# Performance work log

Hardware: AMD Instinct MI355X
Metric: run time of the kernel (lower is better)

The kernel has to match this reference:

```python
import jax, jax.numpy as jnp
import numpy as np

N_ITER = 3


def squash(v):
    # v: [..., out_C]; scale by ||v||^2/(1+||v||^2) and normalize by ||v||
    sq = jnp.sum(v * v, axis=-1, keepdims=True)
    return (sq / (1.0 + sq)) * v / jnp.sqrt(sq)


def setup_inputs() -> dict:
    key = jax.random.key(0)
    k1, k2 = jax.random.split(key)
    B, n_nodes, n_caps, in_C, out_C = 64, 2048, 32, 16, 32
    x = jax.random.normal(k1, (B, n_nodes, in_C), dtype=jnp.float32)
    route_weights = 0.1 * jax.random.normal(k2, (n_nodes, n_caps, in_C, out_C), dtype=jnp.float32)
    return {"x": x, "route_weights": route_weights}


def reference(x, route_weights):
    # priors: [B, n_nodes, n_caps, out_C]
    priors = jnp.einsum('bni,nkio->bnko', x, route_weights)
    logits = jnp.zeros_like(priors)
    outputs = None
    for i in range(N_ITER):
        probs = jax.nn.softmax(logits, axis=2)            # over n_caps
        s = jnp.sum(probs * priors, axis=1, keepdims=True)  # [B,1,n_caps,out_C]
        outputs = squash(s)
        if i != N_ITER - 1:
            delta = jnp.sum(priors * outputs, axis=-1, keepdims=True)
            logits = logits + delta
    return outputs
```

## Files before the change

kernel.cpp:

```cpp
#include <hip/hip_runtime.h>
#include <math.h>


#define BATCH 64
#define NN    2048
#define NK    32
#define NI    16
#define NO    32

#define PNB   16
#define NSETS (NN / PNB)
#define NCH   4
#define XT_JS 528
#define XT0_JS 1040

typedef __bf16 bf16x8 __attribute__((ext_vector_type(8)));
typedef float  f32x16 __attribute__((ext_vector_type(16)));

__device__ __forceinline__ unsigned short f2bf(float f) {
    unsigned int x = __float_as_uint(f);
    unsigned int lsb = (x >> 16) & 1u;
    x += 0x7fffu + lsb;
    return (unsigned short)(x >> 16);
}
__device__ __forceinline__ float bflo(unsigned int u) { return __uint_as_float(u << 16); }
__device__ __forceinline__ float bfhi(unsigned int u) { return __uint_as_float(u & 0xffff0000u); }

__global__ __launch_bounds__(1024) void pass0_fused(
    const float* __restrict__ xg,
    const float* __restrict__ Wg,
    unsigned short* __restrict__ wq,
    float* __restrict__ part)
{
    __shared__ unsigned short xt_lds[PNB * XT0_JS];

    const int tid   = threadIdx.x;
    const int w     = tid >> 6;
    const int lane  = tid & 63;
    const int l5    = lane & 31;
    const int h5    = lane >> 5;
    const int set   = blockIdx.x;
    const int khalf = blockIdx.y;
    const int k     = khalf * 16 + w;
    const int nbase = set * PNB;

#pragma unroll
    for (int rr = 0; rr < 4; ++rr) {
        const int id  = tid + rr * 1024;
        const int bl  = id >> 6;
        const int rem = id & 63;
        const int j   = rem >> 2;
        const int i4  = rem & 3;
        float4 v = *(const float4*)(xg + ((size_t)bl * NN + (nbase + j)) * NI + i4 * 4);
        ushort4 o4;
        o4.x = f2bf(v.x); o4.y = f2bf(v.y); o4.z = f2bf(v.z); o4.w = f2bf(v.w);
        *(ushort4*)(xt_lds + j * XT0_JS + bl * 16 + i4 * 4) = o4;
    }
    __syncthreads();

    float sa0[16], sa1[16];
#pragma unroll
    for (int r = 0; r < 16; ++r) { sa0[r] = 0.f; sa1[r] = 0.f; }

    float wf[8];
    {
        const float* wsrc = Wg + ((size_t)nbase * NK + k) * (NI * NO) + h5 * 8 * NO + l5;
#pragma unroll
        for (int jj = 0; jj < 8; ++jj)
            wf[jj] = wsrc[jj * NO];
    }

    for (int j = 0; j < PNB; ++j) {
        const int n = nbase + j;
        float wfn[8];
        if (j < PNB - 1) {
            const float* wsrcN = Wg + ((size_t)(n + 1) * NK + k) * (NI * NO) + h5 * 8 * NO + l5;
#pragma unroll
            for (int jj = 0; jj < 8; ++jj)
                wfn[jj] = wsrcN[jj * NO];
        }

        unsigned short us[8];
#pragma unroll
        for (int jj = 0; jj < 8; ++jj)
            us[jj] = f2bf(wf[jj]);
        *(uint4*)(wq + ((size_t)n * NK + k) * (NO * NI) + l5 * NI + h5 * 8) = *(uint4*)us;
        const bf16x8 bC = *(const bf16x8*)us;

        const bf16x8 aA = *(const bf16x8*)(xt_lds + j * XT0_JS + l5 * 16 + h5 * 8);
        const bf16x8 aB = *(const bf16x8*)(xt_lds + j * XT0_JS + 512 + l5 * 16 + h5 * 8);

        f32x16 c0, c1;
#pragma unroll
        for (int r = 0; r < 16; ++r) { c0[r] = 0.f; c1[r] = 0.f; }
        c0 = __builtin_amdgcn_mfma_f32_32x32x16_bf16(bC, aA, c0, 0, 0, 0);
        c1 = __builtin_amdgcn_mfma_f32_32x32x16_bf16(bC, aB, c1, 0, 0, 0);
#pragma unroll
        for (int r = 0; r < 16; ++r) { sa0[r] += c0[r]; sa1[r] += c1[r]; }

        if (j < PNB - 1) {
#pragma unroll
            for (int jj = 0; jj < 8; ++jj)
                wf[jj] = wfn[jj];
        }
    }

    float* pb = part + ((size_t)(khalf * NSETS + set) << 15);
#pragma unroll
    for (int r = 0; r < 16; ++r) {
        const int o = (r & 3) + 8 * (r >> 2) + 4 * h5;
        pb[(w * NO + o) * 64 + l5]      = sa0[r] * (1.f / NK);
        pb[(w * NO + o) * 64 + 32 + l5] = sa1[r] * (1.f / NK);
    }
}

template <int PASS>
__global__ __launch_bounds__(1024) void fused_pass(
    const float* __restrict__ xg,
    const unsigned short* __restrict__ wq,
    const float* __restrict__ vpart,
    float* __restrict__ logits0,
    float* __restrict__ part)
{
    __shared__ unsigned short xt_lds[PNB * XT_JS];
    __shared__ float delta_lds[2][32 * 33];

    const int tid  = threadIdx.x;
    const int w    = tid >> 6;
    const int lane = tid & 63;
    const int l5   = lane & 31;
    const int h5   = lane >> 5;
    const int set  = blockIdx.x;
    const int hb   = blockIdx.y;
    const int k0   = 2 * w, k1 = 2 * w + 1;
    const int gb5  = hb * 32 + l5;
    const int sb   = tid >> 5;
    const int sk   = tid & 31;
    const int nbase = set * PNB;

#pragma unroll
    for (int rr = 0; rr < 2; ++rr) {
        const int id  = tid + rr * 1024;
        const int bl  = id >> 6;
        const int rem = id & 63;
        const int j   = rem >> 2;
        const int i4  = rem & 3;
        float4 v = *(const float4*)(xg + ((size_t)(hb * 32 + bl) * NN + (nbase + j)) * NI + i4 * 4);
        ushort4 o4;
        o4.x = f2bf(v.x); o4.y = f2bf(v.y); o4.z = f2bf(v.z); o4.w = f2bf(v.w);
        *(ushort4*)(xt_lds + j * XT_JS + bl * 16 + i4 * 4) = o4;
    }
    __syncthreads();

    unsigned orp0[8], orp1[8];
    {
        float v0[16], v1[16];
        float sq0 = 0.f, sq1 = 0.f;
#pragma unroll
        for (int r = 0; r < 16; ++r) {
            const int o = (r & 3) + 8 * (r >> 2) + 4 * h5;
            float a = 0.f, b = 0.f;
#pragma unroll
            for (int c = 0; c < NCH; ++c) {
                a += vpart[(((size_t)c * NK + k0) * NO + o) * BATCH + gb5];
                b += vpart[(((size_t)c * NK + k1) * NO + o) * BATCH + gb5];
            }
            v0[r] = a; v1[r] = b;
            sq0 = fmaf(a, a, sq0);
            sq1 = fmaf(b, b, sq1);
        }
        sq0 += __shfl_xor(sq0, 32);
        sq1 += __shfl_xor(sq1, 32);
        const float cf0 = sq0 / ((1.f + sq0) * sqrtf(sq0));
        const float cf1 = sq1 / ((1.f + sq1) * sqrtf(sq1));
#pragma unroll
        for (int q = 0; q < 8; ++q) {
            orp0[q] = (unsigned)f2bf(v0[2 * q] * cf0) | ((unsigned)f2bf(v0[2 * q + 1] * cf0) << 16);
            orp1[q] = (unsigned)f2bf(v1[2 * q] * cf1) | ((unsigned)f2bf(v1[2 * q + 1] * cf1) << 16);
        }
    }

    float sa0[16], sa1[16];
#pragma unroll
    for (int r = 0; r < 16; ++r) { sa0[r] = 0.f; sa1[r] = 0.f; }

    bf16x8 b0N, b1N;
    float gN = 0.f;
    {
        const int n = nbase;
        b0N = *(const bf16x8*)(wq + (size_t)n * (NK * NO * NI) + k0 * (NO * NI) + l5 * NI + h5 * 8);
        b1N = *(const bf16x8*)(wq + (size_t)n * (NK * NO * NI) + k1 * (NO * NI) + l5 * NI + h5 * 8);
        if constexpr (PASS == 2)
            gN = logits0[(size_t)n * (BATCH * NK) + hb * 1024 + tid];
    }

    int buf = 0;
    for (int j = 0; j < PNB; ++j) {
        const int n = nbase + j;
        const bf16x8 b0C = b0N, b1C = b1N;
        const float gC = gN;
        if (j < PNB - 1) {
            const int n2 = n + 1;
            b0N = *(const bf16x8*)(wq + (size_t)n2 * (NK * NO * NI) + k0 * (NO * NI) + l5 * NI + h5 * 8);
            b1N = *(const bf16x8*)(wq + (size_t)n2 * (NK * NO * NI) + k1 * (NO * NI) + l5 * NI + h5 * 8);
            if constexpr (PASS == 2)
                gN = logits0[(size_t)n2 * (BATCH * NK) + hb * 1024 + tid];
        }
        const bf16x8 aC = *(const bf16x8*)(xt_lds + j * XT_JS + l5 * 16 + h5 * 8);

        f32x16 c0, c1;
#pragma unroll
        for (int r = 0; r < 16; ++r) { c0[r] = 0.f; c1[r] = 0.f; }
        c0 = __builtin_amdgcn_mfma_f32_32x32x16_bf16(b0C, aC, c0, 0, 0, 0);
        c1 = __builtin_amdgcn_mfma_f32_32x32x16_bf16(b1C, aC, c1, 0, 0, 0);

        float d0 = 0.f, d1 = 0.f;
#pragma unroll
        for (int r = 0; r < 16; ++r) {
            const unsigned u0 = orp0[r >> 1], u1 = orp1[r >> 1];
            const float o0 = (r & 1) ? bfhi(u0) : bflo(u0);
            const float o1 = (r & 1) ? bfhi(u1) : bflo(u1);
            d0 = fmaf(c0[r], o0, d0);
            d1 = fmaf(c1[r], o1, d1);
        }
        d0 += __shfl_xor(d0, 32);
        d1 += __shfl_xor(d1, 32);

        delta_lds[buf][l5 * 33 + (h5 ? k1 : k0)] = h5 ? d1 : d0;
        __syncthreads();

        float l = delta_lds[buf][sb * 33 + sk];
        if constexpr (PASS == 1)
            logits0[(size_t)n * (BATCH * NK) + hb * 1024 + tid] = l;
        else
            l += gC;
        float e = __expf(l);
        float s = e;
#pragma unroll
        for (int mask = 1; mask < 32; mask <<= 1)
            s += __shfl_xor(s, mask);
        delta_lds[buf][sb * 33 + sk] = e / s;
        __syncthreads();

        const float p0 = delta_lds[buf][l5 * 33 + k0];
        const float p1 = delta_lds[buf][l5 * 33 + k1];
#pragma unroll
        for (int r = 0; r < 16; ++r) {
            sa0[r] = fmaf(p0, c0[r], sa0[r]);
            sa1[r] = fmaf(p1, c1[r], sa1[r]);
        }
        buf ^= 1;
    }

    float* pb = part + ((size_t)(hb * NSETS + set) << 15);
#pragma unroll
    for (int r = 0; r < 16; ++r) {
        const int o = (r & 3) + 8 * (r >> 2) + 4 * h5;
        pb[(k0 * NO + o) * 32 + l5] = sa0[r];
        pb[(k1 * NO + o) * 32 + l5] = sa1[r];
    }
}

__global__ __launch_bounds__(1024) void reduce_stageA(
    const float* __restrict__ part,
    float* __restrict__ vpart)
{
    const int k  = blockIdx.x;
    const int hb = blockIdx.y;
    const int c  = blockIdx.z;
    const int t  = threadIdx.x;
    const int o  = t >> 5;
    const int b  = t & 31;

    const float* src = part + ((size_t)(hb * NSETS + c * (NSETS / NCH)) << 15)
                            + (k << 10) + (o << 5) + b;
    float v0 = 0.f, v1 = 0.f, v2 = 0.f, v3 = 0.f;
#pragma unroll 4
    for (int s = 0; s < NSETS / NCH; s += 4) {
        v0 += src[(size_t)(s + 0) << 15];
        v1 += src[(size_t)(s + 1) << 15];
        v2 += src[(size_t)(s + 2) << 15];
        v3 += src[(size_t)(s + 3) << 15];
    }
    vpart[(((size_t)c * NK + k) * NO + o) * BATCH + hb * 32 + b] = (v0 + v1) + (v2 + v3);
}

__global__ __launch_bounds__(1024) void reduce_stageA0(
    const float* __restrict__ part,
    float* __restrict__ vpart)
{
    const int k  = blockIdx.x;
    const int hb = blockIdx.y;
    const int c  = blockIdx.z;
    const int t  = threadIdx.x;
    const int o  = t >> 5;
    const int b  = t & 31;
    const int khalf = k >> 4, kk = k & 15;

    const float* src = part + ((size_t)(khalf * NSETS + c * (NSETS / NCH)) << 15)
                            + ((kk * NO + o) << 6) + hb * 32 + b;
    float v0 = 0.f, v1 = 0.f, v2 = 0.f, v3 = 0.f;
#pragma unroll 4
    for (int s = 0; s < NSETS / NCH; s += 4) {
        v0 += src[(size_t)(s + 0) << 15];
        v1 += src[(size_t)(s + 1) << 15];
        v2 += src[(size_t)(s + 2) << 15];
        v3 += src[(size_t)(s + 3) << 15];
    }
    vpart[(((size_t)c * NK + k) * NO + o) * BATCH + hb * 32 + b] = (v0 + v1) + (v2 + v3);
}

__global__ __launch_bounds__(1024) void reduce_final(
    const float* __restrict__ vpart,
    float* __restrict__ outp)
{
    __shared__ float s_lds[32 * 33];
    __shared__ float cf_lds[32];
    const int k  = blockIdx.x;
    const int hb = blockIdx.y;
    const int t  = threadIdx.x;
    const int o  = t >> 5;
    const int b  = t & 31;

    float v = 0.f;
#pragma unroll
    for (int c = 0; c < NCH; ++c)
        v += vpart[(((size_t)c * NK + k) * NO + o) * BATCH + hb * 32 + b];
    s_lds[o * 33 + b] = v;
    __syncthreads();
    if (t < 32) {
        float sq = 0.f;
#pragma unroll
        for (int oo = 0; oo < 32; ++oo) { const float x = s_lds[oo * 33 + t]; sq = fmaf(x, x, sq); }
        cf_lds[t] = sq / ((1.f + sq) * sqrtf(sq));
    }
    __syncthreads();
    const int bq = t >> 5, oq = t & 31;
    outp[(size_t)(hb * 32 + bq) * 1024 + k * 32 + oq] = s_lds[oq * 33 + bq] * cf_lds[bq];
}


#define LBB 32
#define LNCHUNK 8
#define LNBLK (NN / LNCHUNK)
#define LTHREADS 512
#define WK_STRIDE 516

template <int PASS>
__global__ __launch_bounds__(LTHREADS, 1) void legacy_pass(
    const float* __restrict__ xg, const float* __restrict__ Wg,
    const float* __restrict__ outvL, float* __restrict__ logits,
    float* __restrict__ partial)
{
    __shared__ float w_lds[NK * WK_STRIDE];
    __shared__ float x_lds[LBB][NI + 1];
    __shared__ float delta_lds[LBB][NK + 1];
    const int t = threadIdx.x, nb = blockIdx.x, bg = blockIdx.y;
    const int b0 = bg * LBB;
    const int k = t >> 4, bq = t & 15, bl0 = bq * 2, bl1 = bq * 2 + 1;
    float acc0[NO], acc1[NO];
#pragma unroll
    for (int o = 0; o < NO; ++o) { acc0[o] = 0.f; acc1[o] = 0.f; }
    float outr0[NO], outr1[NO];
    if constexpr (PASS >= 1) {
        const float4* o0 = (const float4*)&outvL[((b0 + bl0) * NK + k) * NO];
        const float4* o1 = (const float4*)&outvL[((b0 + bl1) * NK + k) * NO];
#pragma unroll
        for (int q = 0; q < NO / 4; ++q) {
            float4 a = o0[q]; float4 b = o1[q];
            outr0[4*q+0]=a.x; outr0[4*q+1]=a.y; outr0[4*q+2]=a.z; outr0[4*q+3]=a.w;
            outr1[4*q+0]=b.x; outr1[4*q+1]=b.y; outr1[4*q+2]=b.z; outr1[4*q+3]=b.w;
        }
    }
    for (int j = 0; j < LNCHUNK; ++j) {
        const int n = nb * LNCHUNK + j;
        __syncthreads();
        {
            const float4* src = (const float4*)(Wg + (size_t)n * (NK * NI * NO));
#pragma unroll
            for (int r = 0; r < (NK * NI * NO / 4) / LTHREADS; ++r) {
                int idx4 = t + r * LTHREADS;
                float4 v = src[idx4];
                int e = idx4 * 4, kk = e >> 9, rem = e & 511;
                *(float4*)&w_lds[kk * WK_STRIDE + rem] = v;
            }
        }
        { int bl = t >> 4, i = t & 15;
          x_lds[bl][i] = xg[((size_t)(b0 + bl) * NN + n) * NI + i]; }
        __syncthreads();
        if constexpr (PASS == 0) {
#pragma unroll
            for (int i = 0; i < NI; ++i) {
                float xa = x_lds[bl0][i], xb = x_lds[bl1][i];
                const float* wrow = &w_lds[k * WK_STRIDE + i * NO];
#pragma unroll
                for (int o = 0; o < NO; ++o) {
                    float w = wrow[o];
                    acc0[o] = fmaf(xa, w, acc0[o]);
                    acc1[o] = fmaf(xb, w, acc1[o]);
                }
            }
        } else {
            float pr0[NO], pr1[NO];
#pragma unroll
            for (int o = 0; o < NO; ++o) { pr0[o] = 0.f; pr1[o] = 0.f; }
#pragma unroll
            for (int i = 0; i < NI; ++i) {
                float xa = x_lds[bl0][i], xb = x_lds[bl1][i];
                const float* wrow = &w_lds[k * WK_STRIDE + i * NO];
#pragma unroll
                for (int o = 0; o < NO; ++o) {
                    float w = wrow[o];
                    pr0[o] = fmaf(xa, w, pr0[o]);
                    pr1[o] = fmaf(xb, w, pr1[o]);
                }
            }
            float d0 = 0.f, d1 = 0.f;
#pragma unroll
            for (int o = 0; o < NO; ++o) {
                d0 = fmaf(pr0[o], outr0[o], d0);
                d1 = fmaf(pr1[o], outr1[o], d1);
            }
            float l0 = d0, l1 = d1;
            const size_t li0 = ((size_t)(b0 + bl0) * NN + n) * NK + k;
            const size_t li1 = ((size_t)(b0 + bl1) * NN + n) * NK + k;
            if constexpr (PASS == 2) { l0 += logits[li0]; l1 += logits[li1]; }
            else { logits[li0] = d0; logits[li1] = d1; }
            delta_lds[bl0][k] = l0; delta_lds[bl1][k] = l1;
            __syncthreads();
            float m0 = -1e30f, m1 = -1e30f;
#pragma unroll
            for (int kk = 0; kk < NK; ++kk) {
                m0 = fmaxf(m0, delta_lds[bl0][kk]);
                m1 = fmaxf(m1, delta_lds[bl1][kk]);
            }
            float s0 = 0.f, s1 = 0.f;
#pragma unroll
            for (int kk = 0; kk < NK; ++kk) {
                s0 += __expf(delta_lds[bl0][kk] - m0);
                s1 += __expf(delta_lds[bl1][kk] - m1);
            }
            float p0 = __expf(l0 - m0) / s0;
            float p1 = __expf(l1 - m1) / s1;
#pragma unroll
            for (int o = 0; o < NO; ++o) {
                acc0[o] = fmaf(p0, pr0[o], acc0[o]);
                acc1[o] = fmaf(p1, pr1[o], acc1[o]);
            }
        }
    }
    const float scale = (PASS == 0) ? (1.f / NK) : 1.f;
    float4* p0 = (float4*)&partial[(((size_t)nb * BATCH + (b0 + bl0)) * NK + k) * NO];
    float4* p1 = (float4*)&partial[(((size_t)nb * BATCH + (b0 + bl1)) * NK + k) * NO];
#pragma unroll
    for (int q = 0; q < NO / 4; ++q) {
        float4 v0, v1;
        v0.x = acc0[4*q+0]*scale; v0.y = acc0[4*q+1]*scale;
        v0.z = acc0[4*q+2]*scale; v0.w = acc0[4*q+3]*scale;
        v1.x = acc1[4*q+0]*scale; v1.y = acc1[4*q+1]*scale;
        v1.z = acc1[4*q+2]*scale; v1.w = acc1[4*q+3]*scale;
        p0[q] = v0; p1[q] = v1;
    }
}

__global__ __launch_bounds__(256) void legacy_reduce(
    const float* __restrict__ partial, float* __restrict__ outf)
{
    const int tid = blockIdx.x * 256 + threadIdx.x;
    float v = 0.f;
    for (int nb = 0; nb < LNBLK; ++nb)
        v += partial[(size_t)nb * (BATCH * NK * NO) + tid];
    float sq = v * v;
#pragma unroll
    for (int off = 1; off < 32; off <<= 1) sq += __shfl_xor(sq, off);
    float coef = sq / ((1.f + sq) * sqrtf(sq));
    outf[tid] = v * coef;
}


extern "C" void kernel_launch(void* const* d_in, const int* in_sizes, int n_in,
                              void* d_out, int out_size, void* d_ws, size_t ws_size,
                              hipStream_t stream)
{
    const float* xg = (const float*)d_in[0];
    const float* Wg = (const float*)d_in[1];
    float* outp = (float*)d_out;
    char* ws = (char*)d_ws;

    const size_t SZ_WQ     = (size_t)NN * NK * NO * NI * 2;
    const size_t SZ_PART   = (size_t)256 * 32768 * 4;
    const size_t SZ_LOGITS = (size_t)NN * BATCH * NK * 4;
    const size_t SZ_VPART  = (size_t)NCH * NK * NO * BATCH * 4;
    const size_t NEED = SZ_WQ + SZ_PART + SZ_LOGITS + SZ_VPART;

    if (ws_size >= NEED) {
        unsigned short* wq = (unsigned short*)ws;
        float* part    = (float*)(ws + SZ_WQ);
        float* logits0 = (float*)(ws + SZ_WQ + SZ_PART);
        float* vpart   = (float*)(ws + SZ_WQ + SZ_PART + SZ_LOGITS);

        dim3 pg(NSETS, 2);
        dim3 ra(NK, 2, NCH);
        dim3 fg(NK, 2);
        pass0_fused<<<pg, 1024, 0, stream>>>(xg, Wg, wq, part);
        reduce_stageA0<<<ra, 1024, 0, stream>>>(part, vpart);
        fused_pass<1><<<pg, 1024, 0, stream>>>(xg, wq, vpart, logits0, part);
        reduce_stageA<<<ra, 1024, 0, stream>>>(part, vpart);
        fused_pass<2><<<pg, 1024, 0, stream>>>(xg, wq, vpart, logits0, part);
        reduce_stageA<<<ra, 1024, 0, stream>>>(part, vpart);
        reduce_final<<<fg, 1024, 0, stream>>>(vpart, outp);
    } else {
        float* partial = (float*)ws;
        float* logits = (float*)(ws + (size_t)LNBLK * BATCH * NK * NO * 4);
        float* outvL = (float*)(ws + (size_t)LNBLK * BATCH * NK * NO * 4 + (size_t)BATCH * NN * NK * 4);
        dim3 grid(LNBLK, BATCH / LBB);
        const int rblocks = BATCH * NK * NO / 256;
        legacy_pass<0><<<grid, LTHREADS, 0, stream>>>(xg, Wg, nullptr, logits, partial);
        legacy_reduce<<<rblocks, 256, 0, stream>>>(partial, outvL);
        legacy_pass<1><<<grid, LTHREADS, 0, stream>>>(xg, Wg, outvL, logits, partial);
        legacy_reduce<<<rblocks, 256, 0, stream>>>(partial, outvL);
        legacy_pass<2><<<grid, LTHREADS, 0, stream>>>(xg, Wg, outvL, logits, partial);
        legacy_reduce<<<rblocks, 256, 0, stream>>>(partial, outp);
    }
}
```

Measured before the change: 320.9 us.

## Fuse all routing passes into one persistent kernel with grid barriers

Replaces the seven kernel launches (pass0, reductions, two routing passes, final squash) with a single persistent kernel of 256 blocks that synchronises between stages using atomic grid barriers in workspace memory. The x tile is converted to bf16 and staged in LDS once and reused across all passes, so the per-pass reload goes away. This is meant to cut launch gaps and redundant x loads, at the cost of spin-wait barrier overhead, a reliance on all 256 blocks being co-resident, and an extra memset launch.

```diff
diff --git a/kernel.cpp b/kernel.cpp
--- a/kernel.cpp
+++ b/kernel.cpp
@@ -11,7 +11,7 @@
 #define PNB   16
 #define NSETS (NN / PNB)
 #define NCH   4
-#define XT_JS 528
+#define NBLK  256
 #define XT0_JS 1040
 
 typedef __bf16 bf16x8 __attribute__((ext_vector_type(8)));
@@ -26,22 +26,38 @@
 __device__ __forceinline__ float bflo(unsigned int u) { return __uint_as_float(u << 16); }
 __device__ __forceinline__ float bfhi(unsigned int u) { return __uint_as_float(u & 0xffff0000u); }
 
-__global__ __launch_bounds__(1024) void pass0_fused(
+__device__ __forceinline__ void grid_bar(unsigned* __restrict__ bar, int idx) {
+    __syncthreads();
+    if (threadIdx.x == 0) {
+        __builtin_amdgcn_fence(__ATOMIC_RELEASE, "agent");
+        __hip_atomic_fetch_add(&bar[idx], 1u, __ATOMIC_RELAXED, __HIP_MEMORY_SCOPE_AGENT);
+        while (__hip_atomic_load(&bar[idx], __ATOMIC_RELAXED, __HIP_MEMORY_SCOPE_AGENT) < NBLK)
+            __builtin_amdgcn_s_sleep(2);
+        __builtin_amdgcn_fence(__ATOMIC_ACQUIRE, "agent");
+    }
+    __syncthreads();
+}
+
+__global__ __launch_bounds__(1024) void routing_mega(
     const float* __restrict__ xg,
     const float* __restrict__ Wg,
     unsigned short* __restrict__ wq,
-    float* __restrict__ part)
+    float* __restrict__ part,
+    float* __restrict__ logits0,
+    float* __restrict__ vpart,
+    unsigned* __restrict__ bar,
+    float* __restrict__ outp)
 {
     __shared__ unsigned short xt_lds[PNB * XT0_JS];
-
-    const int tid   = threadIdx.x;
-    const int w     = tid >> 6;
-    const int lane  = tid & 63;
-    const int l5    = lane & 31;
-    const int h5    = lane >> 5;
-    const int set   = blockIdx.x;
-    const int khalf = blockIdx.y;
-    const int k     = khalf * 16 + w;
+    __shared__ float delta_lds[2][32 * 33];
+
+    const int tid  = threadIdx.x;
+    const int bid  = blockIdx.x;
+    const int w    = tid >> 6;
+    const int lane = tid & 63;
+    const int l5   = lane & 31;
+    const int h5   = lane >> 5;
+    const int set  = bid & 127;
     const int nbase = set * PNB;
 
 #pragma unroll
@@ -58,285 +74,248 @@
     }
     __syncthreads();
 
-    float sa0[16], sa1[16];
-#pragma unroll
-    for (int r = 0; r < 16; ++r) { sa0[r] = 0.f; sa1[r] = 0.f; }
-
-    float wf[8];
     {
-        const float* wsrc = Wg + ((size_t)nbase * NK + k) * (NI * NO) + h5 * 8 * NO + l5;
-#pragma unroll
-        for (int jj = 0; jj < 8; ++jj)
-            wf[jj] = wsrc[jj * NO];
-    }
-
-    for (int j = 0; j < PNB; ++j) {
-        const int n = nbase + j;
-        float wfn[8];
-        if (j < PNB - 1) {
-            const float* wsrcN = Wg + ((size_t)(n + 1) * NK + k) * (NI * NO) + h5 * 8 * NO + l5;
-#pragma unroll
-            for (int jj = 0; jj < 8; ++jj)
-                wfn[jj] = wsrcN[jj * NO];
-        }
-
-        unsigned short us[8];
-#pragma unroll
-        for (int jj = 0; jj < 8; ++jj)
-            us[jj] = f2bf(wf[jj]);
-        *(uint4*)(wq + ((size_t)n * NK + k) * (NO * NI) + l5 * NI + h5 * 8) = *(uint4*)us;
-        const bf16x8 bC = *(const bf16x8*)us;
-
-        const bf16x8 aA = *(const bf16x8*)(xt_lds + j * XT0_JS + l5 * 16 + h5 * 8);
-        const bf16x8 aB = *(const bf16x8*)(xt_lds + j * XT0_JS + 512 + l5 * 16 + h5 * 8);
-
-        f32x16 c0, c1;
-#pragma unroll
-        for (int r = 0; r < 16; ++r) { c0[r] = 0.f; c1[r] = 0.f; }
-        c0 = __builtin_amdgcn_mfma_f32_32x32x16_bf16(bC, aA, c0, 0, 0, 0);
-        c1 = __builtin_amdgcn_mfma_f32_32x32x16_bf16(bC, aB, c1, 0, 0, 0);
-#pragma unroll
-        for (int r = 0; r < 16; ++r) { sa0[r] += c0[r]; sa1[r] += c1[r]; }
-
-        if (j < PNB - 1) {
-#pragma unroll
-            for (int jj = 0; jj < 8; ++jj)
-                wf[jj] = wfn[jj];
-        }
-    }
-
-    float* pb = part + ((size_t)(khalf * NSETS + set) << 15);
-#pragma unroll
-    for (int r = 0; r < 16; ++r) {
-        const int o = (r & 3) + 8 * (r >> 2) + 4 * h5;
-        pb[(w * NO + o) * 64 + l5]      = sa0[r] * (1.f / NK);
-        pb[(w * NO + o) * 64 + 32 + l5] = sa1[r] * (1.f / NK);
-    }
-}
-
-template <int PASS>
-__global__ __launch_bounds__(1024) void fused_pass(
-    const float* __restrict__ xg,
-    const unsigned short* __restrict__ wq,
-    const float* __restrict__ vpart,
-    float* __restrict__ logits0,
-    float* __restrict__ part)
-{
-    __shared__ unsigned short xt_lds[PNB * XT_JS];
-    __shared__ float delta_lds[2][32 * 33];
-
-    const int tid  = threadIdx.x;
-    const int w    = tid >> 6;
-    const int lane = tid & 63;
-    const int l5   = lane & 31;
-    const int h5   = lane >> 5;
-    const int set  = blockIdx.x;
-    const int hb   = blockIdx.y;
-    const int k0   = 2 * w, k1 = 2 * w + 1;
-    const int gb5  = hb * 32 + l5;
-    const int sb   = tid >> 5;
-    const int sk   = tid & 31;
-    const int nbase = set * PNB;
-
-#pragma unroll
-    for (int rr = 0; rr < 2; ++rr) {
-        const int id  = tid + rr * 1024;
-        const int bl  = id >> 6;
-        const int rem = id & 63;
-        const int j   = rem >> 2;
-        const int i4  = rem & 3;
-        float4 v = *(const float4*)(xg + ((size_t)(hb * 32 + bl) * NN + (nbase + j)) * NI + i4 * 4);
-        ushort4 o4;
-        o4.x = f2bf(v.x); o4.y = f2bf(v.y); o4.z = f2bf(v.z); o4.w = f2bf(v.w);
-        *(ushort4*)(xt_lds + j * XT_JS + bl * 16 + i4 * 4) = o4;
-    }
-    __syncthreads();
-
-    unsigned orp0[8], orp1[8];
-    {
-        float v0[16], v1[16];
-        float sq0 = 0.f, sq1 = 0.f;
+        const int khalf = bid >> 7;
+        const int k     = khalf * 16 + w;
+
+        float sa0[16], sa1[16];
+#pragma unroll
+        for (int r = 0; r < 16; ++r) { sa0[r] = 0.f; sa1[r] = 0.f; }
+
+        float wf[8];
+        {
+            const float* wsrc = Wg + ((size_t)nbase * NK + k) * (NI * NO) + h5 * 8 * NO + l5;
+#pragma unroll
+            for (int jj = 0; jj < 8; ++jj) wf[jj] = wsrc[jj * NO];
+        }
+
+        for (int j = 0; j < PNB; ++j) {
+            const int n = nbase + j;
+            float wfn[8];
+            if (j < PNB - 1) {
+                const float* wsrcN = Wg + ((size_t)(n + 1) * NK + k) * (NI * NO) + h5 * 8 * NO + l5;
+#pragma unroll
+                for (int jj = 0; jj < 8; ++jj) wfn[jj] = wsrcN[jj * NO];
+            }
+            unsigned short us[8];
+#pragma unroll
+            for (int jj = 0; jj < 8; ++jj) us[jj] = f2bf(wf[jj]);
+            *(uint4*)(wq + ((size_t)n * NK + k) * (NO * NI) + l5 * NI + h5 * 8) = *(uint4*)us;
+            const bf16x8 bC = *(const bf16x8*)us;
+
+            const bf16x8 aA = *(const bf16x8*)(xt_lds + j * XT0_JS + l5 * 16 + h5 * 8);
+            const bf16x8 aB = *(const bf16x8*)(xt_lds + j * XT0_JS + 512 + l5 * 16 + h5 * 8);
+
+            f32x16 c0, c1;
+#pragma unroll
+            for (int r = 0; r < 16; ++r) { c0[r] = 0.f; c1[r] = 0.f; }
+            c0 = __builtin_amdgcn_mfma_f32_32x32x16_bf16(bC, aA, c0, 0, 0, 0);
+            c1 = __builtin_amdgcn_mfma_f32_32x32x16_bf16(bC, aB, c1, 0, 0, 0);
+#pragma unroll
+            for (int r = 0; r < 16; ++r) { sa0[r] += c0[r]; sa1[r] += c1[r]; }
+
+            if (j < PNB - 1) {
+#pragma unroll
+                for (int jj = 0; jj < 8; ++jj) wf[jj] = wfn[jj];
+            }
+        }
+
+        float* pb = part + ((size_t)bid << 15);
 #pragma unroll
         for (int r = 0; r < 16; ++r) {
             const int o = (r & 3) + 8 * (r >> 2) + 4 * h5;
-            float a = 0.f, b = 0.f;
-#pragma unroll
-            for (int c = 0; c < NCH; ++c) {
-                a += vpart[(((size_t)c * NK + k0) * NO + o) * BATCH + gb5];
-                b += vpart[(((size_t)c * NK + k1) * NO + o) * BATCH + gb5];
-            }
-            v0[r] = a; v1[r] = b;
-            sq0 = fmaf(a, a, sq0);
-            sq1 = fmaf(b, b, sq1);
-        }
-        sq0 += __shfl_xor(sq0, 32);
-        sq1 += __shfl_xor(sq1, 32);
-        const float cf0 = sq0 / ((1.f + sq0) * sqrtf(sq0));
-        const float cf1 = sq1 / ((1.f + sq1) * sqrtf(sq1));
-#pragma unroll
-        for (int q = 0; q < 8; ++q) {
-            orp0[q] = (unsigned)f2bf(v0[2 * q] * cf0) | ((unsigned)f2bf(v0[2 * q + 1] * cf0) << 16);
-            orp1[q] = (unsigned)f2bf(v1[2 * q] * cf1) | ((unsigned)f2bf(v1[2 * q + 1] * cf1) << 16);
-        }
-    }
-
-    float sa0[16], sa1[16];
-#pragma unroll
-    for (int r = 0; r < 16; ++r) { sa0[r] = 0.f; sa1[r] = 0.f; }
-
-    bf16x8 b0N, b1N;
-    float gN = 0.f;
+            pb[(w * NO + o) * 64 + l5]      = sa0[r] * (1.f / NK);
+            pb[(w * NO + o) * 64 + 32 + l5] = sa1[r] * (1.f / NK);
+        }
+    }
+    grid_bar(bar, 0);
+
     {
-        const int n = nbase;
-        b0N = *(const bf16x8*)(wq + (size_t)n * (NK * NO * NI) + k0 * (NO * NI) + l5 * NI + h5 * 8);
-        b1N = *(const bf16x8*)(wq + (size_t)n * (NK * NO * NI) + k1 * (NO * NI) + l5 * NI + h5 * 8);
-        if constexpr (PASS == 2)
-            gN = logits0[(size_t)n * (BATCH * NK) + hb * 1024 + tid];
-    }
-
-    int buf = 0;
-    for (int j = 0; j < PNB; ++j) {
-        const int n = nbase + j;
-        const bf16x8 b0C = b0N, b1C = b1N;
-        const float gC = gN;
-        if (j < PNB - 1) {
-            const int n2 = n + 1;
-            b0N = *(const bf16x8*)(wq + (size_t)n2 * (NK * NO * NI) + k0 * (NO * NI) + l5 * NI + h5 * 8);
-            b1N = *(const bf16x8*)(wq + (size_t)n2 * (NK * NO * NI) + k1 * (NO * NI) + l5 * NI + h5 * 8);
-            if constexpr (PASS == 2)
-                gN = logits0[(size_t)n2 * (BATCH * NK) + hb * 1024 + tid];
-        }
-        const bf16x8 aC = *(const bf16x8*)(xt_lds + j * XT_JS + l5 * 16 + h5 * 8);
-
-        f32x16 c0, c1;
-#pragma unroll
-        for (int r = 0; r < 16; ++r) { c0[r] = 0.f; c1[r] = 0.f; }
-        c0 = __builtin_amdgcn_mfma_f32_32x32x16_bf16(b0C, aC, c0, 0, 0, 0);
-        c1 = __builtin_amdgcn_mfma_f32_32x32x16_bf16(b1C, aC, c1, 0, 0, 0);
-
-        float d0 = 0.f, d1 = 0.f;
+        const int k  = bid & 31;
+        const int hb = (bid >> 5) & 1;
+        const int c  = bid >> 6;
+        const int o  = tid >> 5;
+        const int b  = tid & 31;
+        const int khalf = k >> 4, kk = k & 15;
+
+        const float* src = part + ((size_t)(khalf * NSETS + c * (NSETS / NCH)) << 15)
+                                + ((kk * NO + o) << 6) + hb * 32 + b;
+        float v0 = 0.f, v1 = 0.f, v2 = 0.f, v3 = 0.f;
+#pragma unroll 4
+        for (int s = 0; s < NSETS / NCH; s += 4) {
+            v0 += src[(size_t)(s + 0) << 15];
+            v1 += src[(size_t)(s + 1) << 15];
+            v2 += src[(size_t)(s + 2) << 15];
+            v3 += src[(size_t)(s + 3) << 15];
+        }
+        vpart[(((size_t)c * NK + k) * NO + o) * BATCH + hb * 32 + b] = (v0 + v1) + (v2 + v3);
+    }
+    grid_bar(bar, 1);
+
+    const int hb  = bid >> 7;
+    const int k0  = 2 * w, k1 = 2 * w + 1;
+    const int gb5 = hb * 32 + l5;
+    const int sb  = tid >> 5;
+    const int sk  = tid & 31;
+
+#pragma unroll 1
+    for (int pass = 1; pass <= 2; ++pass) {
+        unsigned orp0[8], orp1[8];
+        {
+            float v0[16], v1[16];
+            float sq0 = 0.f, sq1 = 0.f;
+#pragma unroll
+            for (int r = 0; r < 16; ++r) {
+                const int o = (r & 3) + 8 * (r >> 2) + 4 * h5;
+                float a = 0.f, b2 = 0.f;
+#pragma unroll
+                for (int c = 0; c < NCH; ++c) {
+                    a  += vpart[(((size_t)c * NK + k0) * NO + o) * BATCH + gb5];
+                    b2 += vpart[(((size_t)c * NK + k1) * NO + o) * BATCH + gb5];
+                }
+                v0[r] = a; v1[r] = b2;
+                sq0 = fmaf(a, a, sq0);
+                sq1 = fmaf(b2, b2, sq1);
+            }
+            sq0 += __shfl_xor(sq0, 32);
+            sq1 += __shfl_xor(sq1, 32);
+            const float cf0 = sq0 / ((1.f + sq0) * sqrtf(sq0));
+            const float cf1 = sq1 / ((1.f + sq1) * sqrtf(sq1));
+#pragma unroll
+            for (int q = 0; q < 8; ++q) {
+                orp0[q] = (unsigned)f2bf(v0[2 * q] * cf0) | ((unsigned)f2bf(v0[2 * q + 1] * cf0) << 16);
+                orp1[q] = (unsigned)f2bf(v1[2 * q] * cf1) | ((unsigned)f2bf(v1[2 * q + 1] * cf1) << 16);
+            }
+        }
+
+        float sa0[16], sa1[16];
+#pragma unroll
+        for (int r = 0; r < 16; ++r) { sa0[r] = 0.f; sa1[r] = 0.f; }
+
+        bf16x8 b0N, b1N;
+        float gN = 0.f;
+        {
+            const int n = nbase;
+            b0N = *(const bf16x8*)(wq + (size_t)n * (NK * NO * NI) + k0 * (NO * NI) + l5 * NI + h5 * 8);
+            b1N = *(const bf16x8*)(wq + (size_t)n * (NK * NO * NI) + k1 * (NO * NI) + l5 * NI + h5 * 8);
+            if (pass == 2)
+                gN = logits0[(size_t)n * (BATCH * NK) + hb * 1024 + tid];
+        }
+
+        int buf = 0;
+        for (int j = 0; j < PNB; ++j) {
+            const int n = nbase + j;
+            const bf16x8 b0C = b0N, b1C = b1N;
+            const float gC = gN;
+            if (j < PNB - 1) {
+                const int n2 = n + 1;
+                b0N = *(const bf16x8*)(wq + (size_t)n2 * (NK * NO * NI) + k0 * (NO * NI) + l5 * NI + h5 * 8);
+                b1N = *(const bf16x8*)(wq + (size_t)n2 * (NK * NO * NI) + k1 * (NO * NI) + l5 * NI + h5 * 8);
+                if (pass == 2)
+                    gN = logits0[(size_t)n2 * (BATCH * NK) + hb * 1024 + tid];
+            }
+            const bf16x8 aC = *(const bf16x8*)(xt_lds + j * XT0_JS + gb5 * 16 + h5 * 8);
+
+            f32x16 c0, c1;
+#pragma unroll
+            for (int r = 0; r < 16; ++r) { c0[r] = 0.f; c1[r] = 0.f; }
+            c0 = __builtin_amdgcn_mfma_f32_32x32x16_bf16(b0C, aC, c0, 0, 0, 0);
+            c1 = __builtin_amdgcn_mfma_f32_32x32x16_bf16(b1C, aC, c1, 0, 0, 0);
+
+            float d0 = 0.f, d1 = 0.f;
+#pragma unroll
+            for (int r = 0; r < 16; ++r) {
+                const unsigned u0 = orp0[r >> 1], u1 = orp1[r >> 1];
+                const float o0 = (r & 1) ? bfhi(u0) : bflo(u0);
+                const float o1 = (r & 1) ? bfhi(u1) : bflo(u1);
+                d0 = fmaf(c0[r], o0, d0);
+                d1 = fmaf(c1[r], o1, d1);
+            }
+            d0 += __shfl_xor(d0, 32);
+            d1 += __shfl_xor(d1, 32);
+
+            delta_lds[buf][l5 * 33 + (h5 ? k1 : k0)] = h5 ? d1 : d0;
+            __syncthreads();
+
+            float l = delta_lds[buf][sb * 33 + sk];
+            if (pass == 1)
+                logits0[(size_t)n * (BATCH * NK) + hb * 1024 + tid] = l;
+            else
+                l += gC;
+            float e = __expf(l);
+            float s = e;
+#pragma unroll
+            for (int mask = 1; mask < 32; mask <<= 1)
+                s += __shfl_xor(s, mask);
+            delta_lds[buf][sb * 33 + sk] = e / s;
+            __syncthreads();
+
+            const float p0 = delta_lds[buf][l5 * 33 + k0];
+            const float p1 = delta_lds[buf][l5 * 33 + k1];
+#pragma unroll
+            for (int r = 0; r < 16; ++r) {
+                sa0[r] = fmaf(p0, c0[r], sa0[r]);
+                sa1[r] = fmaf(p1, c1[r], sa1[r]);
+            }
+            buf ^= 1;
+        }
+
+        float* pb = part + ((size_t)bid << 15);
 #pragma unroll
         for (int r = 0; r < 16; ++r) {
-            const unsigned u0 = orp0[r >> 1], u1 = orp1[r >> 1];
-            const float o0 = (r & 1) ? bfhi(u0) : bflo(u0);
-            const float o1 = (r & 1) ? bfhi(u1) : bflo(u1);
-            d0 = fmaf(c0[r], o0, d0);
-            d1 = fmaf(c1[r], o1, d1);
-        }
-        d0 += __shfl_xor(d0, 32);
-        d1 += __shfl_xor(d1, 32);
-
-        delta_lds[buf][l5 * 33 + (h5 ? k1 : k0)] = h5 ? d1 : d0;
+            const int o = (r & 3) + 8 * (r >> 2) + 4 * h5;
+            pb[(k0 * NO + o) * 32 + l5] = sa0[r];
+            pb[(k1 * NO + o) * 32 + l5] = sa1[r];
+        }
+
+        grid_bar(bar, 2 * pass);
+
+        {
+            const int k  = bid & 31;
+            const int hb2 = (bid >> 5) & 1;
+            const int c  = bid >> 6;
+            const int o  = tid >> 5;
+            const int b  = tid & 31;
+
+            const float* src = part + ((size_t)(hb2 * NSETS + c * (NSETS / NCH)) << 15)
+                                    + (k << 10) + (o << 5) + b;
+            float v0 = 0.f, v1 = 0.f, v2 = 0.f, v3 = 0.f;
+#pragma unroll 4
+            for (int s = 0; s < NSETS / NCH; s += 4) {
+                v0 += src[(size_t)(s + 0) << 15];
+                v1 += src[(size_t)(s + 1) << 15];
+                v2 += src[(size_t)(s + 2) << 15];
+                v3 += src[(size_t)(s + 3) << 15];
+            }
+            vpart[(((size_t)c * NK + k) * NO + o) * BATCH + hb2 * 32 + b] = (v0 + v1) + (v2 + v3);
+        }
+        grid_bar(bar, 2 * pass + 1);
+    }
+
+    if (bid < 64) {
+        const int k   = bid & 31;
+        const int hbf = bid >> 5;
+        const int o   = tid >> 5;
+        const int b   = tid & 31;
+        float* s_lds  = &delta_lds[0][0];
+        float* cf_lds = &delta_lds[1][0];
+
+        float v = 0.f;
+#pragma unroll
+        for (int c = 0; c < NCH; ++c)
+            v += vpart[(((size_t)c * NK + k) * NO + o) * BATCH + hbf * 32 + b];
+        s_lds[o * 33 + b] = v;
         __syncthreads();
-
-        float l = delta_lds[buf][sb * 33 + sk];
-        if constexpr (PASS == 1)
-            logits0[(size_t)n * (BATCH * NK) + hb * 1024 + tid] = l;
-        else
-            l += gC;
-        float e = __expf(l);
-        float s = e;
-#pragma unroll
-        for (int mask = 1; mask < 32; mask <<= 1)
-            s += __shfl_xor(s, mask);
-        delta_lds[buf][sb * 33 + sk] = e / s;
+        if (tid < 32) {
+            float sq = 0.f;
+#pragma unroll
+            for (int oo = 0; oo < 32; ++oo) { const float x = s_lds[oo * 33 + tid]; sq = fmaf(x, x, sq); }
+            cf_lds[tid] = sq / ((1.f + sq) * sqrtf(sq));
+        }
         __syncthreads();
-
-        const float p0 = delta_lds[buf][l5 * 33 + k0];
-        const float p1 = delta_lds[buf][l5 * 33 + k1];
-#pragma unroll
-        for (int r = 0; r < 16; ++r) {
-            sa0[r] = fmaf(p0, c0[r], sa0[r]);
-            sa1[r] = fmaf(p1, c1[r], sa1[r]);
-        }
-        buf ^= 1;
-    }
-
-    float* pb = part + ((size_t)(hb * NSETS + set) << 15);
-#pragma unroll
-    for (int r = 0; r < 16; ++r) {
-        const int o = (r & 3) + 8 * (r >> 2) + 4 * h5;
-        pb[(k0 * NO + o) * 32 + l5] = sa0[r];
-        pb[(k1 * NO + o) * 32 + l5] = sa1[r];
-    }
-}
-
-__global__ __launch_bounds__(1024) void reduce_stageA(
-    const float* __restrict__ part,
-    float* __restrict__ vpart)
-{
-    const int k  = blockIdx.x;
-    const int hb = blockIdx.y;
-    const int c  = blockIdx.z;
-    const int t  = threadIdx.x;
-    const int o  = t >> 5;
-    const int b  = t & 31;
-
-    const float* src = part + ((size_t)(hb * NSETS + c * (NSETS / NCH)) << 15)
-                            + (k << 10) + (o << 5) + b;
-    float v0 = 0.f, v1 = 0.f, v2 = 0.f, v3 = 0.f;
-#pragma unroll 4
-    for (int s = 0; s < NSETS / NCH; s += 4) {
-        v0 += src[(size_t)(s + 0) << 15];
-        v1 += src[(size_t)(s + 1) << 15];
-        v2 += src[(size_t)(s + 2) << 15];
-        v3 += src[(size_t)(s + 3) << 15];
-    }
-    vpart[(((size_t)c * NK + k) * NO + o) * BATCH + hb * 32 + b] = (v0 + v1) + (v2 + v3);
-}
-
-__global__ __launch_bounds__(1024) void reduce_stageA0(
-    const float* __restrict__ part,
-    float* __restrict__ vpart)
-{
-    const int k  = blockIdx.x;
-    const int hb = blockIdx.y;
-    const int c  = blockIdx.z;
-    const int t  = threadIdx.x;
-    const int o  = t >> 5;
-    const int b  = t & 31;
-    const int khalf = k >> 4, kk = k & 15;
-
-    const float* src = part + ((size_t)(khalf * NSETS + c * (NSETS / NCH)) << 15)
-                            + ((kk * NO + o) << 6) + hb * 32 + b;
-    float v0 = 0.f, v1 = 0.f, v2 = 0.f, v3 = 0.f;
-#pragma unroll 4
-    for (int s = 0; s < NSETS / NCH; s += 4) {
-        v0 += src[(size_t)(s + 0) << 15];
-        v1 += src[(size_t)(s + 1) << 15];
-        v2 += src[(size_t)(s + 2) << 15];
-        v3 += src[(size_t)(s + 3) << 15];
-    }
-    vpart[(((size_t)c * NK + k) * NO + o) * BATCH + hb * 32 + b] = (v0 + v1) + (v2 + v3);
-}
-
-__global__ __launch_bounds__(1024) void reduce_final(
-    const float* __restrict__ vpart,
-    float* __restrict__ outp)
-{
-    __shared__ float s_lds[32 * 33];
-    __shared__ float cf_lds[32];
-    const int k  = blockIdx.x;
-    const int hb = blockIdx.y;
-    const int t  = threadIdx.x;
-    const int o  = t >> 5;
-    const int b  = t & 31;
-
-    float v = 0.f;
-#pragma unroll
-    for (int c = 0; c < NCH; ++c)
-        v += vpart[(((size_t)c * NK + k) * NO + o) * BATCH + hb * 32 + b];
-    s_lds[o * 33 + b] = v;
-    __syncthreads();
-    if (t < 32) {
-        float sq = 0.f;
-#pragma unroll
-        for (int oo = 0; oo < 32; ++oo) { const float x = s_lds[oo * 33 + t]; sq = fmaf(x, x, sq); }
-        cf_lds[t] = sq / ((1.f + sq) * sqrtf(sq));
-    }
-    __syncthreads();
-    const int bq = t >> 5, oq = t & 31;
-    outp[(size_t)(hb * 32 + bq) * 1024 + k * 32 + oq] = s_lds[oq * 33 + bq] * cf_lds[bq];
+        const int bq = tid >> 5, oq = tid & 31;
+        outp[(size_t)(hbf * 32 + bq) * 1024 + k * 32 + oq] = s_lds[oq * 33 + bq] * cf_lds[bq];
+    }
 }
 
 
@@ -491,24 +470,18 @@
     const size_t SZ_PART   = (size_t)256 * 32768 * 4;
     const size_t SZ_LOGITS = (size_t)NN * BATCH * NK * 4;
     const size_t SZ_VPART  = (size_t)NCH * NK * NO * BATCH * 4;
-    const size_t NEED = SZ_WQ + SZ_PART + SZ_LOGITS + SZ_VPART;
+    const size_t SZ_BAR    = 256;
+    const size_t NEED = SZ_WQ + SZ_PART + SZ_LOGITS + SZ_VPART + SZ_BAR;
 
     if (ws_size >= NEED) {
         unsigned short* wq = (unsigned short*)ws;
         float* part    = (float*)(ws + SZ_WQ);
         float* logits0 = (float*)(ws + SZ_WQ + SZ_PART);
         float* vpart   = (float*)(ws + SZ_WQ + SZ_PART + SZ_LOGITS);
-
-        dim3 pg(NSETS, 2);
-        dim3 ra(NK, 2, NCH);
-        dim3 fg(NK, 2);
-        pass0_fused<<<pg, 1024, 0, stream>>>(xg, Wg, wq, part);
-        reduce_stageA0<<<ra, 1024, 0, stream>>>(part, vpart);
-        fused_pass<1><<<pg, 1024, 0, stream>>>(xg, wq, vpart, logits0, part);
-        reduce_stageA<<<ra, 1024, 0, stream>>>(part, vpart);
-        fused_pass<2><<<pg, 1024, 0, stream>>>(xg, wq, vpart, logits0, part);
-        reduce_stageA<<<ra, 1024, 0, stream>>>(part, vpart);
-        reduce_final<<<fg, 1024, 0, stream>>>(vpart, outp);
+        unsigned* bar  = (unsigned*)(ws + SZ_WQ + SZ_PART + SZ_LOGITS + SZ_VPART);
+
+        hipMemsetAsync(bar, 0, 64, stream);
+        routing_mega<<<NBLK, 1024, 0, stream>>>(xg, Wg, wq, part, logits0, vpart, bar, outp);
     } else {
         float* partial = (float*)ws;
         float* logits = (float*)(ws + (size_t)LNBLK * BATCH * NK * NO * 4);
```

Measured after the change: 701.3 us. 2.19x slower.
